# Performance work log

Hardware: AMD Instinct MI355X
Metric: run time of the kernel (lower is better)

## Reference

```python
import jax, jax.numpy as jnp
import numpy as np
from jax import lax

A_MAX = 1.0
ABS_AMIN = 0.0  # a_min = 0.0
B_SZ, L, D_MODEL = 2, 512, 1024
D_INNER, N_STATE, D_CONV, DT_RANK = 2048, 16, 4, 64


def _iso_params(w_pos, w_neg, bias):
    pos_sum = w_pos.sum(axis=1)
    neg_sum = w_neg.sum(axis=1)
    b = bias if bias is not None else jnp.zeros_like(neg_sum)
    b_adj = b - A_MAX * neg_sum - ABS_AMIN * pos_sum
    c = jnp.maximum(-b_adj, 0.0)
    return b_adj + c, c


def _make_iso_linear(key, out_dim, in_dim, with_bias=True):
    kw, kb = jax.random.split(key)
    w = 0.02 * jax.random.normal(kw, (out_dim, in_dim), jnp.float32)
    b = 0.02 * jax.random.normal(kb, (out_dim,), jnp.float32) if with_bias else None
    Wp = jnp.maximum(w, 0.0)
    Wn = jnp.maximum(-w, 0.0)
    bp, c = _iso_params(Wp, Wn, b)
    return Wp, Wn, bp, c


def setup_inputs():
    key = jax.random.key(0)
    ks = jax.random.split(key, 8)
    hidden_states = jax.random.uniform(ks[0], (B_SZ, L, D_MODEL), jnp.float32)
    Win_pos, Win_neg, bin_prime, cin = _make_iso_linear(ks[1], 2 * D_INNER, D_MODEL)
    kw, kb = jax.random.split(ks[2])
    wc = 0.1 * jax.random.normal(kw, (D_INNER, 1, D_CONV), jnp.float32)
    bc = 0.02 * jax.random.normal(kb, (D_INNER,), jnp.float32)
    wc_pos = jnp.maximum(wc, 0.0)
    wc_neg = jnp.maximum(-wc, 0.0)
    bc_prime, cc = _iso_params(wc_pos.reshape(D_INNER, -1), wc_neg.reshape(D_INNER, -1), bc)
    Wx_pos, Wx_neg, bx_prime, cx = _make_iso_linear(ks[3], DT_RANK + 2 * N_STATE, D_INNER, with_bias=False)
    Wdt_pos, Wdt_neg, bdt_prime, cdt = _make_iso_linear(ks[4], D_INNER, DT_RANK, with_bias=False)
    dt_bias = jax.random.uniform(ks[5], (D_INNER,), jnp.float32, -4.0, -2.0)
    dt_c_corr = (Wdt_pos - Wdt_neg) @ cx[:DT_RANK]  # dt_proj.weight @ x_proj.c[:dt_rank]
    Wout_pos, Wout_neg, bout_prime, cout = _make_iso_linear(ks[6], D_MODEL, D_INNER)
    A_log = jnp.log(jnp.broadcast_to(jnp.arange(1, N_STATE + 1, dtype=jnp.float32), (D_INNER, N_STATE)))
    D = jnp.ones((D_INNER,), jnp.float32)
    D_pos = jnp.maximum(D, 0.0)
    D_neg_abs = jnp.maximum(-D, 0.0)
    c_D = ABS_AMIN * D_pos + A_MAX * D_neg_abs
    return dict(hidden_states=hidden_states, Win_pos=Win_pos, Win_neg=Win_neg, bin_prime=bin_prime, cin=cin, wc_pos=wc_pos, wc_neg=wc_neg, bc_prime=bc_prime, cc=cc, Wx_pos=Wx_pos, Wx_neg=Wx_neg, bx_prime=bx_prime, cx=cx, Wdt_pos=Wdt_pos, Wdt_neg=Wdt_neg, bdt_prime=bdt_prime, cdt=cdt, dt_bias=dt_bias, dt_c_corr=dt_c_corr, Wout_pos=Wout_pos, Wout_neg=Wout_neg, bout_prime=bout_prime, cout=cout, A_log=A_log, D_pos=D_pos, D_neg_abs=D_neg_abs, c_D=c_D)


def _iso_lin(x, Wp, Wn, bp, c):
    # IsomorphicLinear: W_pos @ (x + |a_min|) + W_neg_abs @ (a_max - x) + b' - c == W @ x + b
    return (x + ABS_AMIN) @ Wp.T + (A_MAX - x) @ Wn.T + bp - c


def _dw_conv(x, w):
    # depthwise 1D conv, valid padding; x: (b, d, L'), w: (d, 1, k)
    return lax.conv_general_dilated(x, w, (1,), 'VALID', dimension_numbers=('NCH', 'OIH', 'NCH'), feature_group_count=D_INNER)


def reference(hidden_states, Win_pos, Win_neg, bin_prime, cin, wc_pos, wc_neg, bc_prime, cc, Wx_pos, Wx_neg, bx_prime, cx, Wdt_pos, Wdt_neg, bdt_prime, cdt, dt_bias, dt_c_corr, Wout_pos, Wout_neg, bout_prime, cout, A_log, D_pos, D_neg_abs, c_D):
    b, l, dm = hidden_states.shape
    # in_proj -> (b, 2*d_inner, l)
    xz = _iso_lin(hidden_states.reshape(b * l, dm), Win_pos, Win_neg, bin_prime, cin)
    xz = xz.reshape(b, l, 2 * D_INNER).transpose(0, 2, 1)
    x, z = xz[:, :D_INNER], xz[:, D_INNER:]
    x = jnp.clip(x, 0.0, A_MAX)  # LinearBounded at 'in_proj' site
    # IsomorphicConv1D (depthwise, causal pad then truncate to seqlen)
    p = D_CONV - 1
    xp = jnp.pad(x + ABS_AMIN, ((0, 0), (0, 0), (p, p)), constant_values=ABS_AMIN)
    ax = jnp.pad(A_MAX - x, ((0, 0), (0, 0), (p, p)), constant_values=A_MAX)
    y_nn = _dw_conv(xp, wc_pos) + _dw_conv(ax, wc_neg) + bc_prime[None, :, None]
    x = jax.nn.silu((y_nn - cc[None, :, None])[:, :, :l])
    x = jnp.clip(x, 0.0, A_MAX)  # LinearBounded at 'conv' site
    # x_proj: keep non-negative output y_nn (c subtracted per-slice below)
    xf = x.transpose(0, 2, 1).reshape(b * l, D_INNER)
    ynn_x = (xf + ABS_AMIN) @ Wx_pos.T + (A_MAX - xf) @ Wx_neg.T + bx_prime
    dt_nn = ynn_x[:, :DT_RANK]
    Bnn = ynn_x[:, DT_RANK:DT_RANK + N_STATE].reshape(b, l, N_STATE).transpose(0, 2, 1)  # (b, n, l)
    Cnn = ynn_x[:, DT_RANK + N_STATE:].reshape(b, l, N_STATE).transpose(0, 2, 1)
    c_B = cx[DT_RANK:DT_RANK + N_STATE]
    c_C = cx[DT_RANK + N_STATE:]
    # dt_proj (no bias in iso layer) on non-neg dt_nn; correct by W_dt @ c_dt, add real bias
    dt = _iso_lin(dt_nn, Wdt_pos, Wdt_neg, bdt_prime, cdt)
    delta = jax.nn.softplus(dt - dt_c_corr + dt_bias).reshape(b, l, D_INNER).transpose(0, 2, 1)  # (b, d, l)
    # isomorphic selective scan with dual hidden state
    A = jnp.exp(A_log)
    dA = jnp.exp(-jnp.einsum('bdl,dn->lbdn', delta, A))
    dBu = jnp.einsum('bdl,bnl,bdl->lbdn', delta, Bnn, x)
    dcu = (delta * x).transpose(2, 0, 1)[..., None] * c_B  # (l, b, d, n)
    Ct = Cnn.transpose(2, 0, 1)  # (l, b, n)
    h0 = jnp.zeros((b, D_INNER, N_STATE), jnp.float32)

    def step(carry, inp):
        hp, hd = carry
        dA_i, dBu_i, dcu_i, C_i = inp
        hp = dA_i * hp + dBu_i
        hd = dA_i * hd + dcu_i
        y_p = jnp.einsum('bn,bdn->bd', C_i, hp)
        y1 = jnp.einsum('bn,bdn->bd', C_i, hd)
        y2 = jnp.einsum('n,bdn->bd', c_C, hp)
        y3 = jnp.einsum('n,bdn->bd', c_C, hd)
        return (hp, hd), y_p - (y1 + y2 - y3)

    _, ys = lax.scan(step, (h0, h0), (dA, dBu, dcu, Ct))
    y = jnp.moveaxis(ys, 0, 2)  # (b, d_inner, l)
    # isomorphic D skip: D*u = D_pos*(u+|a_min|) + D_neg*(a_max-u) - c_D
    y = y + D_pos[:, None] * (x + ABS_AMIN) + D_neg_abs[:, None] * (A_MAX - x) - c_D[:, None]
    y = jnp.clip(y, 0.0, A_MAX)  # LinearBounded at 'ssm' site
    y = y * jax.nn.silu(z)
    out = _iso_lin(y.transpose(0, 2, 1).reshape(b * l, D_INNER), Wout_pos, Wout_neg, bout_prime, cout)
    return out.reshape(b, l, dm)
```

## Files before the change

### kernel.cpp

```cpp
#include <hip/hip_runtime.h>
#include <math.h>

#define DI 2048
#define NS 16
#define NCHUNK 16
#define CS 32
#define NKC 16

typedef _Float16 half_t;
typedef __attribute__((ext_vector_type(8))) _Float16 half8v;
typedef __attribute__((ext_vector_type(4))) _Float16 half4v;
typedef __attribute__((ext_vector_type(4))) float f32x4;

__device__ __forceinline__ void gload_lds16(const half_t* g, half_t* l) {
    __builtin_amdgcn_global_load_lds(
        (const __attribute__((address_space(1))) unsigned int*)g,
        (__attribute__((address_space(3))) unsigned int*)l, 16, 0, 0);
}

#define JB_WIN   0
#define JB_WOUT  4096
#define JB_WX    5120
#define JB_WDT   5216
#define JB_CONV  5728
#define JB_HID   5736
#define JB_END   6760

__device__ __forceinline__ float block_sum256(float s, int tid, float* red) {
    #pragma unroll
    for (int o = 32; o > 0; o >>= 1) s += __shfl_down(s, o);
    if ((tid & 63) == 0) red[tid >> 6] = s;
    __syncthreads();
    return red[0] + red[1] + red[2] + red[3];
}

__global__ __launch_bounds__(256) void megaprep_kernel(
    const float* __restrict__ hidden,
    const float* __restrict__ Win_pos, const float* __restrict__ Win_neg,
    const float* __restrict__ bin_prime, const float* __restrict__ cin,
    const float* __restrict__ wc_pos, const float* __restrict__ wc_neg,
    const float* __restrict__ bc_prime, const float* __restrict__ cc,
    const float* __restrict__ Wx_pos, const float* __restrict__ Wx_neg,
    const float* __restrict__ bx_prime,
    const float* __restrict__ Wdt_pos, const float* __restrict__ Wdt_neg,
    const float* __restrict__ bdt_prime, const float* __restrict__ cdt,
    const float* __restrict__ Wout_pos, const float* __restrict__ Wout_neg,
    const float* __restrict__ bout_prime, const float* __restrict__ cout,
    half_t* __restrict__ Win_h, float* __restrict__ bin_eff,
    half_t* __restrict__ Wout_h, float* __restrict__ bout_eff,
    half_t* __restrict__ Wx_h, float* __restrict__ bx_eff,
    float* __restrict__ Wdt_eff, float* __restrict__ bdt_eff,
    float* __restrict__ wce, float* __restrict__ cbconv,
    half_t* __restrict__ hid_h)
{
    __shared__ float red[4];
    int b = blockIdx.x, tid = threadIdx.x;

    if (b < JB_WOUT) {
        int r = b;
        size_t base = (size_t)r * 1024 + tid * 4;
        float4 p = *(const float4*)(Win_pos + base);
        float4 n = *(const float4*)(Win_neg + base);
        half4v h;
        h[0] = (half_t)(p.x - n.x); h[1] = (half_t)(p.y - n.y);
        h[2] = (half_t)(p.z - n.z); h[3] = (half_t)(p.w - n.w);
        *(half4v*)(Win_h + base) = h;
        float s = block_sum256(n.x + n.y + n.z + n.w, tid, red);
        if (tid == 0) bin_eff[r] = s + bin_prime[r] - cin[r];
    } else if (b < JB_WX) {
        int r = b - JB_WOUT;
        float s = 0.f;
        #pragma unroll
        for (int j = 0; j < 2; ++j) {
            size_t base = (size_t)r * 2048 + j * 1024 + tid * 4;
            float4 p = *(const float4*)(Wout_pos + base);
            float4 n = *(const float4*)(Wout_neg + base);
            half4v h;
            h[0] = (half_t)(p.x - n.x); h[1] = (half_t)(p.y - n.y);
            h[2] = (half_t)(p.z - n.z); h[3] = (half_t)(p.w - n.w);
            *(half4v*)(Wout_h + base) = h;
            s += n.x + n.y + n.z + n.w;
        }
        s = block_sum256(s, tid, red);
        if (tid == 0) bout_eff[r] = s + bout_prime[r] - cout[r];
    } else if (b < JB_WDT) {
        int r = b - JB_WX;
        float s = 0.f;
        #pragma unroll
        for (int j = 0; j < 2; ++j) {
            size_t base = (size_t)r * 2048 + j * 1024 + tid * 4;
            float4 p = *(const float4*)(Wx_pos + base);
            float4 n = *(const float4*)(Wx_neg + base);
            half4v h;
            h[0] = (half_t)(p.x - n.x); h[1] = (half_t)(p.y - n.y);
            h[2] = (half_t)(p.z - n.z); h[3] = (half_t)(p.w - n.w);
            *(half4v*)(Wx_h + base) = h;
            s += n.x + n.y + n.z + n.w;
        }
        s = block_sum256(s, tid, red);
        if (tid == 0) bx_eff[r] = s + bx_prime[r];
    } else if (b < JB_CONV) {
        int wave = tid >> 6, lane = tid & 63;
        int r = (b - JB_WDT) * 4 + wave;
        float p = Wdt_pos[r * 64 + lane], n = Wdt_neg[r * 64 + lane];
        Wdt_eff[r * 64 + lane] = p - n;
        float s = n;
        #pragma unroll
        for (int o = 32; o > 0; o >>= 1) s += __shfl_down(s, o);
        if (lane == 0) bdt_eff[r] = s + bdt_prime[r] - cdt[r];
    } else if (b < JB_HID) {
        int d = (b - JB_CONV) * 256 + tid;
        float s = 0.f;
        #pragma unroll
        for (int k = 0; k < 4; ++k) {
            float p = wc_pos[d * 4 + k], n = wc_neg[d * 4 + k];
            wce[d * 4 + k] = p - n;
            s += n;
        }
        cbconv[d] = s + bc_prime[d] - cc[d];
    } else {
        size_t i4 = ((size_t)(b - JB_HID) * 256 + tid) * 4;
        float4 x = *(const float4*)(hidden + i4);
        half4v h;
        h[0] = (half_t)x.x; h[1] = (half_t)x.y; h[2] = (half_t)x.z; h[3] = (half_t)x.w;
        *(half4v*)(hid_h + i4) = h;
    }
}


template<int BM, int BN>
__global__ __launch_bounds__(256) void gemm_mfma_3buf(
    const half_t* __restrict__ A, const half_t* __restrict__ Wh,
    const float* __restrict__ bias, float* __restrict__ C, int K, int ldc)
{
    constexpr int MF = BM / 32, NF = BN / 32;
    constexpr int ROWS = BM + BN;
    constexpr int GRP = ROWS / 8;
    __shared__ half_t lds[3][ROWS * 64];

    int tid = threadIdx.x;
    int lane = tid & 63, wv = tid >> 6;
    int wm = (wv >> 1) * (BM / 2);
    int wn = (wv & 1) * (BN / 2);
    int r15 = lane & 15, g4 = lane >> 4;
    int m0 = blockIdx.y * BM, n0 = blockIdx.x * BN;
    int lrow8 = lane >> 3;
    int scol = ((lane & 7) ^ lrow8) << 3;

    f32x4 acc[MF][NF];
    #pragma unroll
    for (int i = 0; i < MF; ++i)
        #pragma unroll
        for (int j = 0; j < NF; ++j)
            acc[i][j] = (f32x4){0.f, 0.f, 0.f, 0.f};

    auto STAGE = [&](int buf, int kt) {
        #pragma unroll
        for (int i = 0; i < GRP / 4; ++i) {
            int g = wv + i * 4;
            const half_t* src; int rb;
            if (g < BM / 8) { src = A;  rb = m0 + g * 8; }
            else            { src = Wh; rb = n0 + (g - BM / 8) * 8; }
            gload_lds16(src + (size_t)(rb + lrow8) * K + kt + scol,
                        &lds[buf][g * 512]);
        }
    };

    int nt = K / 64;
    STAGE(0, 0);
    STAGE(1, 64);
    asm volatile("s_waitcnt vmcnt(4)" ::: "memory");
    __builtin_amdgcn_s_barrier();

    for (int t = 0; t < nt; ++t) {
        if (t + 2 < nt) STAGE((t + 2) % 3, (t + 2) * 64);
        const half_t* lb = &lds[t % 3][0];
        #pragma unroll
        for (int kk = 0; kk < 2; ++kk) {
            half8v af[MF], wh[NF];
            int swz = (((kk << 2) + g4) ^ (r15 & 7)) << 3;
            #pragma unroll
            for (int fm = 0; fm < MF; ++fm)
                af[fm] = *(const half8v*)&lb[(wm + fm * 16 + r15) * 64 + swz];
            #pragma unroll
            for (int fn = 0; fn < NF; ++fn)
                wh[fn] = *(const half8v*)&lb[(BM + wn + fn * 16 + r15) * 64 + swz];
            #pragma unroll
            for (int fm = 0; fm < MF; ++fm)
                #pragma unroll
                for (int fn = 0; fn < NF; ++fn)
                    acc[fm][fn] = __builtin_amdgcn_mfma_f32_16x16x32_f16(af[fm], wh[fn], acc[fm][fn], 0, 0, 0);
        }
        if (t + 2 < nt) { asm volatile("s_waitcnt vmcnt(4)" ::: "memory"); }
        else            { asm volatile("s_waitcnt vmcnt(0)" ::: "memory"); }
        __builtin_amdgcn_s_barrier();
    }

    #pragma unroll
    for (int fm = 0; fm < MF; ++fm)
        #pragma unroll
        for (int fn = 0; fn < NF; ++fn) {
            int col = n0 + wn + fn * 16 + r15;
            float bv = bias[col];
            #pragma unroll
            for (int i = 0; i < 4; ++i) {
                int row = m0 + wm + fm * 16 + g4 * 4 + i;
                C[(size_t)row * ldc + col] = acc[fm][fn][i] + bv;
            }
        }
}


__global__ __launch_bounds__(512) void convgemm2_kernel(
    const float* __restrict__ xzb, const float* __restrict__ wce,
    const float* __restrict__ cbconv, const half_t* __restrict__ Wx_h,
    float* __restrict__ xconv, float* __restrict__ g2part)
{
    __shared__ __align__(16) unsigned char SMEM[40960];
    int tid = threadIdx.x;
    int lane = tid & 63;
    int eng = tid >> 8, etid = tid & 255;
    unsigned char* elds = SMEM + eng * 20480;

    int mt = blockIdx.y, kc = blockIdx.x;
    int m0 = mt * 64;
    int dd0 = kc * 128 + eng * 64;
    half_t* Alds = (half_t*)elds;
    half_t* Wlds = (half_t*)elds + 64 * 64;

    {
        int wv = etid >> 6;
        int lrow8 = lane >> 3;
        int scolw = ((lane & 7) ^ lrow8) << 3;
        #pragma unroll
        for (int i = 0; i < 3; ++i) {
            int g = wv + i * 4;
            gload_lds16(Wx_h + (size_t)(g * 8 + lrow8) * 2048 + dd0 + scolw,
                        Wlds + g * 512);
        }
    }
    {
        int cgp = etid & 7, rr = etid >> 3;
        int dbase = dd0 + cgp * 8;
        float wv_[8][4], cbv[8];
        #pragma unroll
        for (int c = 0; c < 8; ++c) {
            float4 wf = *(const float4*)(wce + (dbase + c) * 4);
            wv_[c][0] = wf.x; wv_[c][1] = wf.y; wv_[c][2] = wf.z; wv_[c][3] = wf.w;
            cbv[c] = cbconv[dbase + c];
        }
        int tl0 = (mt & 7) * 64;
        float xwin[5][8];
        #pragma unroll
        for (int j = 0; j < 5; ++j) {
            int lr = 2 * rr + j - 3;
            if (tl0 + lr >= 0) {
                size_t ixx = (size_t)(m0 + lr) * 4096 + dbase;
                float4 a = *(const float4*)(xzb + ixx);
                float4 b = *(const float4*)(xzb + ixx + 4);
                xwin[j][0] = fminf(fmaxf(a.x, 0.f), 1.f);
                xwin[j][1] = fminf(fmaxf(a.y, 0.f), 1.f);
                xwin[j][2] = fminf(fmaxf(a.z, 0.f), 1.f);
                xwin[j][3] = fminf(fmaxf(a.w, 0.f), 1.f);
                xwin[j][4] = fminf(fmaxf(b.x, 0.f), 1.f);
                xwin[j][5] = fminf(fmaxf(b.y, 0.f), 1.f);
                xwin[j][6] = fminf(fmaxf(b.z, 0.f), 1.f);
                xwin[j][7] = fminf(fmaxf(b.w, 0.f), 1.f);
            } else {
                #pragma unroll
                for (int c = 0; c < 8; ++c) xwin[j][c] = 0.f;
            }
        }
        #pragma unroll
        for (int q = 0; q < 2; ++q) {
            int row = 2 * rr + q;
            float outv[8];
            #pragma unroll
            for (int c = 0; c < 8; ++c) {
                float a = cbv[c];
                #pragma unroll
                for (int k = 0; k < 4; ++k) a = fmaf(wv_[c][k], xwin[q + k][c], a);
                float s = a / (1.f + __expf(-a));
                outv[c] = fminf(fmaxf(s, 0.f), 1.f);
            }
            size_t ox = (size_t)(m0 + row) * 2048 + dbase;
            *(float4*)(xconv + ox)     = make_float4(outv[0], outv[1], outv[2], outv[3]);
            *(float4*)(xconv + ox + 4) = make_float4(outv[4], outv[5], outv[6], outv[7]);
            half8v hv;
            #pragma unroll
            for (int c = 0; c < 8; ++c) hv[c] = (half_t)outv[c];
            *(half8v*)&Alds[row * 64 + ((cgp ^ (row & 7)) << 3)] = hv;
        }
    }
    __syncthreads();
    int wv = etid >> 6;
    int wm = (wv >> 1) * 32, wn = (wv & 1) * 48;
    int r15 = lane & 15, g4 = lane >> 4;
    f32x4 acc2[2][3];
    #pragma unroll
    for (int i = 0; i < 2; ++i)
        #pragma unroll
        for (int j = 0; j < 3; ++j) acc2[i][j] = (f32x4){0.f, 0.f, 0.f, 0.f};
    #pragma unroll
    for (int kk = 0; kk < 2; ++kk) {
        int swz = (((kk << 2) + g4) ^ (r15 & 7)) << 3;
        half8v af[2], wh[3];
        #pragma unroll
        for (int fm = 0; fm < 2; ++fm)
            af[fm] = *(const half8v*)&Alds[(wm + fm * 16 + r15) * 64 + swz];
        #pragma unroll
        for (int fn = 0; fn < 3; ++fn)
            wh[fn] = *(const half8v*)&Wlds[(wn + fn * 16 + r15) * 64 + swz];
        #pragma unroll
        for (int fm = 0; fm < 2; ++fm)
            #pragma unroll
            for (int fn = 0; fn < 3; ++fn)
                acc2[fm][fn] = __builtin_amdgcn_mfma_f32_16x16x32_f16(af[fm], wh[fn], acc2[fm][fn], 0, 0, 0);
    }
    __syncthreads();
    float* comb = (float*)SMEM;
    if (eng == 1) {
        #pragma unroll
        for (int fm = 0; fm < 2; ++fm)
            #pragma unroll
            for (int fn = 0; fn < 3; ++fn)
                #pragma unroll
                for (int i = 0; i < 4; ++i)
                    comb[etid * 24 + (fm * 3 + fn) * 4 + i] = acc2[fm][fn][i];
    }
    __syncthreads();
    if (eng == 0) {
        #pragma unroll
        for (int fm = 0; fm < 2; ++fm)
            #pragma unroll
            for (int fn = 0; fn < 3; ++fn) {
                int col = wn + fn * 16 + r15;
                #pragma unroll
                for (int i = 0; i < 4; ++i) {
                    int row = m0 + wm + fm * 16 + g4 * 4 + i;
                    float v = acc2[fm][fn][i] + comb[etid * 24 + (fm * 3 + fn) * 4 + i];
                    g2part[((size_t)kc * 1024 + row) * 96 + col] = v;
                }
            }
    }
}


__global__ __launch_bounds__(256) void gemm3_kernel(
    const float* __restrict__ g2part, const float* __restrict__ bx_eff,
    const float* __restrict__ Bw, const float* __restrict__ bias,
    const float* __restrict__ e1, const float* __restrict__ e2,
    float* __restrict__ delta)
{
    __shared__ float As[16][68];
    __shared__ float Bs[16][68];
    int tid = threadIdx.x;
    int tx = tid & 15, ty = tid >> 4;
    int m0 = blockIdx.y * 64, n0 = blockIdx.x * 64;
    int lr = tid >> 2;
    int lk = (tid & 3) << 2;
    float acc[4][4] = {};
    const float* Bptr = Bw + (size_t)(n0 + lr) * 64 + lk;

    for (int kt = 0; kt < 64; kt += 16) {
        float4 av = *(const float4*)(bx_eff + kt + lk);
        #pragma unroll
        for (int c = 0; c < NKC; ++c) {
            float4 pv = *(const float4*)(g2part + (size_t)c * 98304 + (size_t)(m0 + lr) * 96 + kt + lk);
            av.x += pv.x; av.y += pv.y; av.z += pv.z; av.w += pv.w;
        }
        float4 bv = *(const float4*)(Bptr + kt);
        __syncthreads();
        As[lk + 0][lr] = av.x; As[lk + 1][lr] = av.y; As[lk + 2][lr] = av.z; As[lk + 3][lr] = av.w;
        Bs[lk + 0][lr] = bv.x; Bs[lk + 1][lr] = bv.y; Bs[lk + 2][lr] = bv.z; Bs[lk + 3][lr] = bv.w;
        __syncthreads();
        #pragma unroll
        for (int k = 0; k < 16; ++k) {
            float4 a4 = *(const float4*)&As[k][ty << 2];
            float4 b4 = *(const float4*)&Bs[k][tx << 2];
            float ar[4] = {a4.x, a4.y, a4.z, a4.w};
            float br[4] = {b4.x, b4.y, b4.z, b4.w};
            #pragma unroll
            for (int i = 0; i < 4; ++i)
                #pragma unroll
                for (int j = 0; j < 4; ++j)
                    acc[i][j] = fmaf(ar[i], br[j], acc[i][j]);
        }
    }

    #pragma unroll
    for (int i = 0; i < 4; ++i) {
        int row = m0 + (ty << 2) + i;
        #pragma unroll
        for (int j = 0; j < 4; ++j) {
            int col = n0 + (tx << 2) + j;
            float v = acc[i][j] + bias[col] - e1[col] + e2[col];
            v = fmaxf(v, 0.f) + log1pf(__expf(-fabsf(v)));
            delta[(size_t)row * 2048 + col] = v;
        }
    }
}


__global__ __launch_bounds__(256) void scan1_kernel(
    const float* __restrict__ delta, const float* __restrict__ xconv,
    const float* __restrict__ g2part, const float* __restrict__ bx_eff,
    const float* __restrict__ cx,
    float* __restrict__ Pbuf, float* __restrict__ Hloc)
{
    __shared__ float bcB[CS][NS];
    int tid = threadIdx.x;
    int c = blockIdx.x;
    int db = blockIdx.y;
    int b = blockIdx.z;
    int d = db * 256 + tid;
    int t0 = c * CS;

    for (int i = tid; i < CS * NS; i += 256) {
        int tt = i >> 4, j = i & 15;
        size_t col = (size_t)(b * 512 + t0 + tt) * 96 + 64 + j;
        float v = bx_eff[64 + j] - cx[64 + j];
        #pragma unroll
        for (int cc = 0; cc < NKC; ++cc) v += g2part[(size_t)cc * 98304 + col];
        bcB[tt][j] = v;
    }
    __syncthreads();

    float h[NS];
    #pragma unroll
    for (int n = 0; n < NS; ++n) h[n] = 0.f;
    float p1 = 1.f;

    const int BT = 8;
    size_t base = (size_t)(b * 512 + t0) * 2048 + d;
    float dltA[BT], xvA[BT];
    #pragma unroll
    for (int j = 0; j < BT; ++j) { dltA[j] = delta[base + j * 2048]; xvA[j] = xconv[base + j * 2048]; }

    for (int bt = 0; bt < CS / BT; ++bt) {
        float dltN[BT], xvN[BT];
        if (bt + 1 < CS / BT) {
            #pragma unroll
            for (int j = 0; j < BT; ++j) {
                size_t o2 = base + (size_t)((bt + 1) * BT + j) * 2048;
                dltN[j] = delta[o2]; xvN[j] = xconv[o2];
            }
        }
        #pragma unroll
        for (int j = 0; j < BT; ++j) {
            int tp = bt * BT + j;
            float dlt = dltA[j], xv = xvA[j];
            float du = dlt * xv;
            float e1 = __expf(-dlt);
            p1 *= e1;
            float dA = 1.f;
            #pragma unroll
            for (int n = 0; n < NS; ++n) {
                dA *= e1;
                h[n] = fmaf(dA, h[n], du * bcB[tp][n]);
            }
        }
        #pragma unroll
        for (int j = 0; j < BT; ++j) { dltA[j] = dltN[j]; xvA[j] = xvN[j]; }
    }

    size_t o = ((size_t)(c * 2 + b) * 2048 + d) * NS;
    float pv[NS];
    float pp = 1.f;
    #pragma unroll
    for (int n = 0; n < NS; ++n) { pp *= p1; pv[n] = pp; }
    #pragma unroll
    for (int q = 0; q < 4; ++q) {
        *(f32x4*)&Pbuf[o + q * 4] = (f32x4){pv[q*4], pv[q*4+1], pv[q*4+2], pv[q*4+3]};
        *(f32x4*)&Hloc[o + q * 4] = (f32x4){h[q*4], h[q*4+1], h[q*4+2], h[q*4+3]};
    }
}

__global__ __launch_bounds__(256) void scan3_kernel(
    const float* __restrict__ delta, const float* __restrict__ xconv,
    const float* __restrict__ g2part, const float* __restrict__ bx_eff,
    const float* __restrict__ cx, const float* __restrict__ xz,
    const float* __restrict__ Dpos, const float* __restrict__ Dneg,
    const float* __restrict__ cD,
    const float* __restrict__ Pbuf, const float* __restrict__ Hloc,
    half_t* __restrict__ y_h)
{
    __shared__ float bc[CS][32];
    int tid = threadIdx.x;
    int c = blockIdx.x;
    int db = blockIdx.y;
    int b = blockIdx.z;
    int d = db * 256 + tid;
    int t0 = c * CS;

    for (int i = tid; i < CS * 32; i += 256) {
        int tt = i >> 5, j = i & 31;
        size_t col = (size_t)(b * 512 + t0 + tt) * 96 + 64 + j;
        float v = bx_eff[64 + j] - cx[64 + j];
        #pragma unroll
        for (int cc = 0; cc < NKC; ++cc) v += g2part[(size_t)cc * 98304 + col];
        bc[tt][j] = v;
    }
    __syncthreads();

    float h[NS];
    #pragma unroll
    for (int n = 0; n < NS; ++n) h[n] = 0.f;
    for (int cc2 = 0; cc2 < c; ++cc2) {
        size_t oo = ((size_t)(cc2 * 2 + b) * 2048 + d) * NS;
        f32x4 P[4], H[4];
        #pragma unroll
        for (int q = 0; q < 4; ++q) {
            P[q] = *(const f32x4*)&Pbuf[oo + q * 4];
            H[q] = *(const f32x4*)&Hloc[oo + q * 4];
        }
        #pragma unroll
        for (int n = 0; n < NS; ++n)
            h[n] = fmaf(P[n >> 2][n & 3], h[n], H[n >> 2][n & 3]);
    }

    float dp = Dpos[d], dn = Dneg[d], cd = cD[d];

    const int BT = 8;
    size_t base = (size_t)(b * 512 + t0) * 2048 + d;
    float dltA[BT], xvA[BT], zA[BT];
    #pragma unroll
    for (int j = 0; j < BT; ++j) {
        dltA[j] = delta[base + j * 2048];
        xvA[j]  = xconv[base + j * 2048];
        zA[j]   = xz[(size_t)(b * 512 + t0 + j) * 4096 + 2048 + d];
    }

    for (int bt = 0; bt < CS / BT; ++bt) {
        float dltN[BT], xvN[BT], zN[BT];
        if (bt + 1 < CS / BT) {
            #pragma unroll
            for (int j = 0; j < BT; ++j) {
                int tp = (bt + 1) * BT + j;
                dltN[j] = delta[base + (size_t)tp * 2048];
                xvN[j]  = xconv[base + (size_t)tp * 2048];
                zN[j]   = xz[(size_t)(b * 512 + t0 + tp) * 4096 + 2048 + d];
            }
        }
        #pragma unroll
        for (int j = 0; j < BT; ++j) {
            int tp = bt * BT + j;
            float dlt = dltA[j], xv = xvA[j];
            float du = dlt * xv;
            float e1 = __expf(-dlt);
            float y = 0.f;
            float dA = 1.f;
            #pragma unroll
            for (int n = 0; n < NS; ++n) {
                dA *= e1;
                h[n] = fmaf(dA, h[n], du * bc[tp][n]);
                y = fmaf(bc[tp][16 + n], h[n], y);
            }
            y += dp * xv + dn * (1.f - xv) - cd;
            y = fminf(fmaxf(y, 0.f), 1.f);
            float z = zA[j];
            y *= z / (1.f + __expf(-z));
            y_h[base + (size_t)tp * 2048] = (half_t)y;
        }
        #pragma unroll
        for (int j = 0; j < BT; ++j) { dltA[j] = dltN[j]; xvA[j] = xvN[j]; zA[j] = zN[j]; }
    }
}


extern "C" void kernel_launch(void* const* d_in, const int* in_sizes, int n_in,
                              void* d_out, int out_size, void* d_ws, size_t ws_size,
                              hipStream_t stream) {
    const float* hidden    = (const float*)d_in[0];
    const float* Win_pos   = (const float*)d_in[1];
    const float* Win_neg   = (const float*)d_in[2];
    const float* bin_prime = (const float*)d_in[3];
    const float* cin       = (const float*)d_in[4];
    const float* wc_pos    = (const float*)d_in[5];
    const float* wc_neg    = (const float*)d_in[6];
    const float* bc_prime  = (const float*)d_in[7];
    const float* cc        = (const float*)d_in[8];
    const float* Wx_pos    = (const float*)d_in[9];
    const float* Wx_neg    = (const float*)d_in[10];
    const float* bx_prime  = (const float*)d_in[11];
    const float* cx        = (const float*)d_in[12];
    const float* Wdt_pos   = (const float*)d_in[13];
    const float* Wdt_neg   = (const float*)d_in[14];
    const float* bdt_prime = (const float*)d_in[15];
    const float* cdt       = (const float*)d_in[16];
    const float* dt_bias   = (const float*)d_in[17];
    const float* dt_c_corr = (const float*)d_in[18];
    const float* Wout_pos  = (const float*)d_in[19];
    const float* Wout_neg  = (const float*)d_in[20];
    const float* bout_prime= (const float*)d_in[21];
    const float* cout      = (const float*)d_in[22];
    const float* D_pos     = (const float*)d_in[24];
    const float* D_neg     = (const float*)d_in[25];
    const float* c_D       = (const float*)d_in[26];
    float* out = (float*)d_out;

    size_t off = 0;
    auto alloc = [&](size_t bytes) { char* p = (char*)d_ws + off; off += (bytes + 4095) & ~(size_t)4095; return (void*)p; };
    half_t* Win_h   = (half_t*)alloc((size_t)4096 * 1024 * 2);
    half_t* Wout_h  = (half_t*)alloc((size_t)1024 * 2048 * 2);
    half_t* Wx_h    = (half_t*)alloc((size_t)96 * 2048 * 2);
    half_t* hid_h   = (half_t*)alloc((size_t)1024 * 1024 * 2);
    half_t* y_h     = (half_t*)alloc((size_t)1024 * 2048 * 2);
    float* bin_eff  = (float*)alloc(4096 * 4);
    float* bx_eff   = (float*)alloc(96 * 4);
    float* Wdt_eff  = (float*)alloc((size_t)2048 * 64 * 4);
    float* bdt_eff  = (float*)alloc(2048 * 4);
    float* bout_eff = (float*)alloc(1024 * 4);
    float* wce      = (float*)alloc(2048 * 4 * 4);
    float* cbconv   = (float*)alloc(2048 * 4);
    float* xzb      = (float*)alloc((size_t)1024 * 4096 * 4);
    float* xconv    = (float*)alloc((size_t)1024 * 2048 * 4);
    float* g2part   = (float*)alloc((size_t)NKC * 1024 * 96 * 4);
    float* delta    = (float*)alloc((size_t)1024 * 2048 * 4);
    float* Pbuf     = (float*)alloc((size_t)NCHUNK * 65536 * 4);
    float* Hloc     = (float*)alloc((size_t)NCHUNK * 65536 * 4);

    megaprep_kernel<<<JB_END, 256, 0, stream>>>(
        hidden, Win_pos, Win_neg, bin_prime, cin,
        wc_pos, wc_neg, bc_prime, cc,
        Wx_pos, Wx_neg, bx_prime,
        Wdt_pos, Wdt_neg, bdt_prime, cdt,
        Wout_pos, Wout_neg, bout_prime, cout,
        Win_h, bin_eff, Wout_h, bout_eff,
        Wx_h, bx_eff, Wdt_eff, bdt_eff, wce, cbconv, hid_h);

    gemm_mfma_3buf<64, 64><<<dim3(64, 16), 256, 0, stream>>>(
        hid_h, Win_h, bin_eff, xzb, 1024, 4096);
    convgemm2_kernel<<<dim3(16, 16), 512, 0, stream>>>(
        xzb, wce, cbconv, Wx_h, xconv, g2part);
    gemm3_kernel<<<dim3(32, 16), 256, 0, stream>>>(g2part, bx_eff, Wdt_eff, bdt_eff,
                                                   dt_c_corr, dt_bias, delta);
    scan1_kernel<<<dim3(NCHUNK, 8, 2), 256, 0, stream>>>(delta, xconv, g2part, bx_eff,
                                                         cx, Pbuf, Hloc);
    scan3_kernel<<<dim3(NCHUNK, 8, 2), 256, 0, stream>>>(delta, xconv, g2part, bx_eff,
                                                         cx, xzb, D_pos, D_neg, c_D,
                                                         Pbuf, Hloc, y_h);
    gemm_mfma_3buf<64, 64><<<dim3(16, 16), 256, 0, stream>>>(
        y_h, Wout_h, bout_eff, out, 2048, 1024);
}
```

Baseline: 106.5 us.

## Fuse dt projection and softplus into scan1, drop separate gemm3 kernel

Removes the standalone dt-projection GEMM kernel and computes delta inside scan1: each block reduces the g2part partials for its chunk's dt-rank rows into LDS, then each thread does a 64-deep dot product per timestep using a transposed Wdt written by the prep kernel. Softplus is applied in place, and delta is written out for scan3 while being kept in registers for the local scan. This saves one launch and one global round trip of delta into scan1. In exchange, scan1 now does extra FMA work and holds larger register arrays (32 xv plus 32 delta values), which may lower occupancy.

```diff
diff --git a/kernel.cpp b/kernel.cpp
--- a/kernel.cpp
+++ b/kernel.cpp
@@ -49,7 +49,7 @@
     half_t* __restrict__ Win_h, float* __restrict__ bin_eff,
     half_t* __restrict__ Wout_h, float* __restrict__ bout_eff,
     half_t* __restrict__ Wx_h, float* __restrict__ bx_eff,
-    float* __restrict__ Wdt_eff, float* __restrict__ bdt_eff,
+    float* __restrict__ WdtT, float* __restrict__ bdt_eff,
     float* __restrict__ wce, float* __restrict__ cbconv,
     half_t* __restrict__ hid_h)
 {
@@ -103,7 +103,7 @@
         int wave = tid >> 6, lane = tid & 63;
         int r = (b - JB_WDT) * 4 + wave;
         float p = Wdt_pos[r * 64 + lane], n = Wdt_neg[r * 64 + lane];
-        Wdt_eff[r * 64 + lane] = p - n;
+        WdtT[(size_t)lane * 2048 + r] = p - n;
         float s = n;
         #pragma unroll
         for (int o = 32; o > 0; o >>= 1) s += __shfl_down(s, o);
@@ -346,68 +346,16 @@
 }
 
 
-__global__ __launch_bounds__(256) void gemm3_kernel(
-    const float* __restrict__ g2part, const float* __restrict__ bx_eff,
-    const float* __restrict__ Bw, const float* __restrict__ bias,
-    const float* __restrict__ e1, const float* __restrict__ e2,
-    float* __restrict__ delta)
-{
-    __shared__ float As[16][68];
-    __shared__ float Bs[16][68];
-    int tid = threadIdx.x;
-    int tx = tid & 15, ty = tid >> 4;
-    int m0 = blockIdx.y * 64, n0 = blockIdx.x * 64;
-    int lr = tid >> 2;
-    int lk = (tid & 3) << 2;
-    float acc[4][4] = {};
-    const float* Bptr = Bw + (size_t)(n0 + lr) * 64 + lk;
-
-    for (int kt = 0; kt < 64; kt += 16) {
-        float4 av = *(const float4*)(bx_eff + kt + lk);
-        #pragma unroll
-        for (int c = 0; c < NKC; ++c) {
-            float4 pv = *(const float4*)(g2part + (size_t)c * 98304 + (size_t)(m0 + lr) * 96 + kt + lk);
-            av.x += pv.x; av.y += pv.y; av.z += pv.z; av.w += pv.w;
-        }
-        float4 bv = *(const float4*)(Bptr + kt);
-        __syncthreads();
-        As[lk + 0][lr] = av.x; As[lk + 1][lr] = av.y; As[lk + 2][lr] = av.z; As[lk + 3][lr] = av.w;
-        Bs[lk + 0][lr] = bv.x; Bs[lk + 1][lr] = bv.y; Bs[lk + 2][lr] = bv.z; Bs[lk + 3][lr] = bv.w;
-        __syncthreads();
-        #pragma unroll
-        for (int k = 0; k < 16; ++k) {
-            float4 a4 = *(const float4*)&As[k][ty << 2];
-            float4 b4 = *(const float4*)&Bs[k][tx << 2];
-            float ar[4] = {a4.x, a4.y, a4.z, a4.w};
-            float br[4] = {b4.x, b4.y, b4.z, b4.w};
-            #pragma unroll
-            for (int i = 0; i < 4; ++i)
-                #pragma unroll
-                for (int j = 0; j < 4; ++j)
-                    acc[i][j] = fmaf(ar[i], br[j], acc[i][j]);
-        }
-    }
-
-    #pragma unroll
-    for (int i = 0; i < 4; ++i) {
-        int row = m0 + (ty << 2) + i;
-        #pragma unroll
-        for (int j = 0; j < 4; ++j) {
-            int col = n0 + (tx << 2) + j;
-            float v = acc[i][j] + bias[col] - e1[col] + e2[col];
-            v = fmaxf(v, 0.f) + log1pf(__expf(-fabsf(v)));
-            delta[(size_t)row * 2048 + col] = v;
-        }
-    }
-}
-
-
 __global__ __launch_bounds__(256) void scan1_kernel(
-    const float* __restrict__ delta, const float* __restrict__ xconv,
+    const float* __restrict__ xconv,
     const float* __restrict__ g2part, const float* __restrict__ bx_eff,
     const float* __restrict__ cx,
+    const float* __restrict__ WdtT, const float* __restrict__ bdt_eff,
+    const float* __restrict__ dt_c_corr, const float* __restrict__ dt_bias,
+    float* __restrict__ delta,
     float* __restrict__ Pbuf, float* __restrict__ Hloc)
 {
+    __shared__ float Aly[CS][64];
     __shared__ float bcB[CS][NS];
     int tid = threadIdx.x;
     int c = blockIdx.x;
@@ -416,52 +364,67 @@
     int d = db * 256 + tid;
     int t0 = c * CS;
 
-    for (int i = tid; i < CS * NS; i += 256) {
-        int tt = i >> 4, j = i & 15;
-        size_t col = (size_t)(b * 512 + t0 + tt) * 96 + 64 + j;
-        float v = bx_eff[64 + j] - cx[64 + j];
-        #pragma unroll
-        for (int cc = 0; cc < NKC; ++cc) v += g2part[(size_t)cc * 98304 + col];
-        bcB[tt][j] = v;
+    size_t base = (size_t)(b * 512 + t0) * 2048 + d;
+    float xv[CS];
+    #pragma unroll
+    for (int t = 0; t < CS; ++t) xv[t] = xconv[base + (size_t)t * 2048];
+
+    for (int i = tid; i < CS * 24; i += 256) {
+        int tt = i / 24, j4 = i % 24;
+        size_t col = (size_t)(b * 512 + t0 + tt) * 96 + j4 * 4;
+        float4 v = *(const float4*)(bx_eff + j4 * 4);
+        if (j4 >= 16) {
+            float4 cv = *(const float4*)(cx + j4 * 4);
+            v.x -= cv.x; v.y -= cv.y; v.z -= cv.z; v.w -= cv.w;
+        }
+        #pragma unroll
+        for (int cc = 0; cc < NKC; ++cc) {
+            float4 pv = *(const float4*)(g2part + (size_t)cc * 98304 + col);
+            v.x += pv.x; v.y += pv.y; v.z += pv.z; v.w += pv.w;
+        }
+        if (j4 < 16) {
+            *(float4*)&Aly[tt][j4 * 4] = v;
+        } else {
+            *(float4*)&bcB[tt][(j4 - 16) * 4] = v;
+        }
     }
     __syncthreads();
+
+    float delt[CS];
+    #pragma unroll
+    for (int t = 0; t < CS; ++t) delt[t] = 0.f;
+    for (int k = 0; k < 64; ++k) {
+        float w = WdtT[(size_t)k * 2048 + d];
+        #pragma unroll
+        for (int t = 0; t < CS; ++t)
+            delt[t] = fmaf(Aly[t][k], w, delt[t]);
+    }
+    {
+        float b0 = bdt_eff[d], e1v = dt_c_corr[d], e2v = dt_bias[d];
+        #pragma unroll
+        for (int t = 0; t < CS; ++t) {
+            float v = delt[t] + b0 - e1v + e2v;
+            v = fmaxf(v, 0.f) + log1pf(__expf(-fabsf(v)));
+            delt[t] = v;
+            delta[base + (size_t)t * 2048] = v;
+        }
+    }
 
     float h[NS];
     #pragma unroll
     for (int n = 0; n < NS; ++n) h[n] = 0.f;
     float p1 = 1.f;
-
-    const int BT = 8;
-    size_t base = (size_t)(b * 512 + t0) * 2048 + d;
-    float dltA[BT], xvA[BT];
-    #pragma unroll
-    for (int j = 0; j < BT; ++j) { dltA[j] = delta[base + j * 2048]; xvA[j] = xconv[base + j * 2048]; }
-
-    for (int bt = 0; bt < CS / BT; ++bt) {
-        float dltN[BT], xvN[BT];
-        if (bt + 1 < CS / BT) {
-            #pragma unroll
-            for (int j = 0; j < BT; ++j) {
-                size_t o2 = base + (size_t)((bt + 1) * BT + j) * 2048;
-                dltN[j] = delta[o2]; xvN[j] = xconv[o2];
-            }
-        }
-        #pragma unroll
-        for (int j = 0; j < BT; ++j) {
-            int tp = bt * BT + j;
-            float dlt = dltA[j], xv = xvA[j];
-            float du = dlt * xv;
-            float e1 = __expf(-dlt);
-            p1 *= e1;
-            float dA = 1.f;
-            #pragma unroll
-            for (int n = 0; n < NS; ++n) {
-                dA *= e1;
-                h[n] = fmaf(dA, h[n], du * bcB[tp][n]);
-            }
-        }
-        #pragma unroll
-        for (int j = 0; j < BT; ++j) { dltA[j] = dltN[j]; xvA[j] = xvN[j]; }
+    #pragma unroll
+    for (int tp = 0; tp < CS; ++tp) {
+        float du = delt[tp] * xv[tp];
+        float e1 = __expf(-delt[tp]);
+        p1 *= e1;
+        float dA = 1.f;
+        #pragma unroll
+        for (int n = 0; n < NS; ++n) {
+            dA *= e1;
+            h[n] = fmaf(dA, h[n], du * bcB[tp][n]);
+        }
     }
 
     size_t o = ((size_t)(c * 2 + b) * 2048 + d) * NS;
@@ -608,7 +571,7 @@
     half_t* y_h     = (half_t*)alloc((size_t)1024 * 2048 * 2);
     float* bin_eff  = (float*)alloc(4096 * 4);
     float* bx_eff   = (float*)alloc(96 * 4);
-    float* Wdt_eff  = (float*)alloc((size_t)2048 * 64 * 4);
+    float* WdtT     = (float*)alloc((size_t)64 * 2048 * 4);
     float* bdt_eff  = (float*)alloc(2048 * 4);
     float* bout_eff = (float*)alloc(1024 * 4);
     float* wce      = (float*)alloc(2048 * 4 * 4);
@@ -627,16 +590,15 @@
         Wdt_pos, Wdt_neg, bdt_prime, cdt,
         Wout_pos, Wout_neg, bout_prime, cout,
         Win_h, bin_eff, Wout_h, bout_eff,
-        Wx_h, bx_eff, Wdt_eff, bdt_eff, wce, cbconv, hid_h);
+        Wx_h, bx_eff, WdtT, bdt_eff, wce, cbconv, hid_h);
 
     gemm_mfma_3buf<64, 64><<<dim3(64, 16), 256, 0, stream>>>(
         hid_h, Win_h, bin_eff, xzb, 1024, 4096);
     convgemm2_kernel<<<dim3(16, 16), 512, 0, stream>>>(
         xzb, wce, cbconv, Wx_h, xconv, g2part);
-    gemm3_kernel<<<dim3(32, 16), 256, 0, stream>>>(g2part, bx_eff, Wdt_eff, bdt_eff,
-                                                   dt_c_corr, dt_bias, delta);
-    scan1_kernel<<<dim3(NCHUNK, 8, 2), 256, 0, stream>>>(delta, xconv, g2part, bx_eff,
-                                                         cx, Pbuf, Hloc);
+    scan1_kernel<<<dim3(NCHUNK, 8, 2), 256, 0, stream>>>(
+        xconv, g2part, bx_eff, cx, WdtT, bdt_eff, dt_c_corr, dt_bias,
+        delta, Pbuf, Hloc);
     scan3_kernel<<<dim3(NCHUNK, 8, 2), 256, 0, stream>>>(delta, xconv, g2part, bx_eff,
                                                          cx, xzb, D_pos, D_neg, c_D,
                                                          Pbuf, Hloc, y_h);
```

After: 106.5 us. About the same (-0.0%).
